# Optimization experiments

Measured on AMD Instinct MI355X. Metric: run time of the kernel, lower is better.

The kernel has to match this reference:

```python
import jax, jax.numpy as jnp
import numpy as np

EPS = 1e-4

def setup_inputs() -> dict:
    key = jax.random.key(0)
    x = jax.random.normal(key, (32, 512, 4000), dtype=jnp.float32)
    return {"x": x}

def reference(x):
    # x: [batch, bins, frames]; causal cumulative normalization along frames
    frames = x.shape[-1]
    count = jnp.arange(1, frames + 1, dtype=x.dtype).reshape(1, 1, frames)
    cum_sum = jnp.cumsum(x, axis=-1)
    cum_pow_sum = jnp.cumsum(x * x, axis=-1)
    cum_mean = cum_sum / count
    cum_var = cum_pow_sum / count - cum_mean * cum_mean
    cum_std = jnp.sqrt(cum_var + EPS)
    return (x - cum_mean) / cum_std
```

## Files before the change

### kernel.cpp

```cpp
#include <hip/hip_runtime.h>

#define EPS 1e-4f
#define FRAMES 4000

__global__ __launch_bounds__(256) void cumnorm_kernel(const float* __restrict__ x,
                                                      float* __restrict__ out,
                                                      int rows) {
    const int wavesPerBlock = blockDim.x >> 6;
    const int row  = blockIdx.x * wavesPerBlock + (threadIdx.x >> 6);
    const int lane = threadIdx.x & 63;
    if (row >= rows) return;

    const float4* __restrict__ xr = (const float4*)(x + (size_t)row * FRAMES);
    float4* __restrict__ outr     = (float4*)(out + (size_t)row * FRAMES);

    const int nvec = FRAMES >> 2;
    float carry_s = 0.0f, carry_q = 0.0f;

    for (int base = 0; base < nvec; base += 64) {
        const int idx = base + lane;
        float4 v = make_float4(0.0f, 0.0f, 0.0f, 0.0f);
        if (idx < nvec) v = xr[idx];

        float s0 = v.x;
        float s1 = s0 + v.y;
        float s2 = s1 + v.z;
        float s3 = s2 + v.w;
        float q0 = v.x * v.x;
        float q1 = fmaf(v.y, v.y, q0);
        float q2 = fmaf(v.z, v.z, q1);
        float q3 = fmaf(v.w, v.w, q2);

        float ss = s3, qq = q3;
        #pragma unroll
        for (int d = 1; d < 64; d <<= 1) {
            float us = __shfl_up(ss, d, 64);
            float uq = __shfl_up(qq, d, 64);
            if (lane >= d) { ss += us; qq += uq; }
        }

        const float tot_s = __shfl(ss, 63, 64);
        const float tot_q = __shfl(qq, 63, 64);

        const float excl_s = (ss - s3) + carry_s;
        const float excl_q = (qq - q3) + carry_q;

        if (idx < nvec) {
            const float base_cnt = (float)(idx << 2);
            float4 r;
            {
                const float cs = excl_s + s0, cq = excl_q + q0;
                const float inv  = __builtin_amdgcn_rcpf(base_cnt + 1.0f);
                const float mean = cs * inv;
                const float var  = fmaf(-mean, mean, cq * inv);
                r.x = (v.x - mean) * __builtin_amdgcn_rsqf(var + EPS);
            }
            {
                const float cs = excl_s + s1, cq = excl_q + q1;
                const float inv  = __builtin_amdgcn_rcpf(base_cnt + 2.0f);
                const float mean = cs * inv;
                const float var  = fmaf(-mean, mean, cq * inv);
                r.y = (v.y - mean) * __builtin_amdgcn_rsqf(var + EPS);
            }
            {
                const float cs = excl_s + s2, cq = excl_q + q2;
                const float inv  = __builtin_amdgcn_rcpf(base_cnt + 3.0f);
                const float mean = cs * inv;
                const float var  = fmaf(-mean, mean, cq * inv);
                r.z = (v.z - mean) * __builtin_amdgcn_rsqf(var + EPS);
            }
            {
                const float cs = excl_s + s3, cq = excl_q + q3;
                const float inv  = __builtin_amdgcn_rcpf(base_cnt + 4.0f);
                const float mean = cs * inv;
                const float var  = fmaf(-mean, mean, cq * inv);
                r.w = (v.w - mean) * __builtin_amdgcn_rsqf(var + EPS);
            }
            outr[idx] = r;
        }

        carry_s += tot_s;
        carry_q += tot_q;
    }
}

extern "C" void kernel_launch(void* const* d_in, const int* in_sizes, int n_in,
                              void* d_out, int out_size, void* d_ws, size_t ws_size,
                              hipStream_t stream) {
    const float* x = (const float*)d_in[0];
    float* out = (float*)d_out;
    const int rows = in_sizes[0] / FRAMES;

    const int block = 256;
    const int rowsPerBlock = block / 64;
    const int grid = (rows + rowsPerBlock - 1) / rowsPerBlock;
    cumnorm_kernel<<<grid, block, 0, stream>>>(x, out, rows);
}
```

Baseline: 432.6 us.

## Scan each row with a whole block using per-thread register chunks

Switches from one wave per row looping over 16 serial chunks to one 256-thread block per row. Each of the 250 active threads loads 16 contiguous elements, does a local serial sum, then a wave shuffle scan plus a shared-memory cross-wave combine. This removes the serial chunk loop and its carried dependency and exposes more memory parallelism per row. In exchange it adds a block barrier, leaves 6 threads idle, and has each thread load four contiguous float4s, which is a strided pattern across lanes.

```diff
diff --git a/kernel.cpp b/kernel.cpp
--- a/kernel.cpp
+++ b/kernel.cpp
@@ -2,85 +2,98 @@
 
 #define EPS 1e-4f
 #define FRAMES 4000
+#define TPB 256
+#define VPT 4
+#define EPT (VPT * 4)
+#define ACTIVE_T (FRAMES / EPT)
 
-__global__ __launch_bounds__(256) void cumnorm_kernel(const float* __restrict__ x,
+__global__ __launch_bounds__(TPB) void cumnorm_kernel(const float* __restrict__ x,
                                                       float* __restrict__ out,
                                                       int rows) {
-    const int wavesPerBlock = blockDim.x >> 6;
-    const int row  = blockIdx.x * wavesPerBlock + (threadIdx.x >> 6);
-    const int lane = threadIdx.x & 63;
+    const int row  = blockIdx.x;
     if (row >= rows) return;
+    const int t    = threadIdx.x;
+    const int wave = t >> 6;
+    const int lane = t & 63;
 
     const float4* __restrict__ xr = (const float4*)(x + (size_t)row * FRAMES);
     float4* __restrict__ outr     = (float4*)(out + (size_t)row * FRAMES);
 
-    const int nvec = FRAMES >> 2;
-    float carry_s = 0.0f, carry_q = 0.0f;
+    const bool active = (t < ACTIVE_T);
 
-    for (int base = 0; base < nvec; base += 64) {
-        const int idx = base + lane;
-        float4 v = make_float4(0.0f, 0.0f, 0.0f, 0.0f);
-        if (idx < nvec) v = xr[idx];
+    float4 v[VPT];
+    if (active) {
+        #pragma unroll
+        for (int j = 0; j < VPT; ++j) v[j] = xr[t * VPT + j];
+    } else {
+        #pragma unroll
+        for (int j = 0; j < VPT; ++j) v[j] = make_float4(0.f, 0.f, 0.f, 0.f);
+    }
 
-        float s0 = v.x;
-        float s1 = s0 + v.y;
-        float s2 = s1 + v.z;
-        float s3 = s2 + v.w;
-        float q0 = v.x * v.x;
-        float q1 = fmaf(v.y, v.y, q0);
-        float q2 = fmaf(v.z, v.z, q1);
-        float q3 = fmaf(v.w, v.w, q2);
+    float S = 0.f, Q = 0.f;
+    #pragma unroll
+    for (int j = 0; j < VPT; ++j) {
+        S += v[j].x; Q = fmaf(v[j].x, v[j].x, Q);
+        S += v[j].y; Q = fmaf(v[j].y, v[j].y, Q);
+        S += v[j].z; Q = fmaf(v[j].z, v[j].z, Q);
+        S += v[j].w; Q = fmaf(v[j].w, v[j].w, Q);
+    }
 
-        float ss = s3, qq = q3;
+    float ss = S, qq = Q;
+    #pragma unroll
+    for (int d = 1; d < 64; d <<= 1) {
+        const float us = __shfl_up(ss, d, 64);
+        const float uq = __shfl_up(qq, d, 64);
+        if (lane >= d) { ss += us; qq += uq; }
+    }
+
+    __shared__ float wsum[4];
+    __shared__ float wsq[4];
+    if (lane == 63) { wsum[wave] = ss; wsq[wave] = qq; }
+    __syncthreads();
+
+    float cs = ss - S;
+    float cq = qq - Q;
+    #pragma unroll
+    for (int w = 0; w < 3; ++w) {
+        if (w < wave) { cs += wsum[w]; cq += wsq[w]; }
+    }
+
+    if (active) {
+        const float nbase = (float)(t * EPT);
         #pragma unroll
-        for (int d = 1; d < 64; d <<= 1) {
-            float us = __shfl_up(ss, d, 64);
-            float uq = __shfl_up(qq, d, 64);
-            if (lane >= d) { ss += us; qq += uq; }
-        }
-
-        const float tot_s = __shfl(ss, 63, 64);
-        const float tot_q = __shfl(qq, 63, 64);
-
-        const float excl_s = (ss - s3) + carry_s;
-        const float excl_q = (qq - q3) + carry_q;
-
-        if (idx < nvec) {
-            const float base_cnt = (float)(idx << 2);
+        for (int j = 0; j < VPT; ++j) {
             float4 r;
             {
-                const float cs = excl_s + s0, cq = excl_q + q0;
-                const float inv  = __builtin_amdgcn_rcpf(base_cnt + 1.0f);
+                cs += v[j].x; cq = fmaf(v[j].x, v[j].x, cq);
+                const float inv  = __builtin_amdgcn_rcpf(nbase + (float)(j * 4 + 1));
                 const float mean = cs * inv;
                 const float var  = fmaf(-mean, mean, cq * inv);
-                r.x = (v.x - mean) * __builtin_amdgcn_rsqf(var + EPS);
+                r.x = (v[j].x - mean) * __builtin_amdgcn_rsqf(var + EPS);
             }
             {
-                const float cs = excl_s + s1, cq = excl_q + q1;
-                const float inv  = __builtin_amdgcn_rcpf(base_cnt + 2.0f);
+                cs += v[j].y; cq = fmaf(v[j].y, v[j].y, cq);
+                const float inv  = __builtin_amdgcn_rcpf(nbase + (float)(j * 4 + 2));
                 const float mean = cs * inv;
                 const float var  = fmaf(-mean, mean, cq * inv);
-                r.y = (v.y - mean) * __builtin_amdgcn_rsqf(var + EPS);
+                r.y = (v[j].y - mean) * __builtin_amdgcn_rsqf(var + EPS);
             }
             {
-                const float cs = excl_s + s2, cq = excl_q + q2;
-                const float inv  = __builtin_amdgcn_rcpf(base_cnt + 3.0f);
+                cs += v[j].z; cq = fmaf(v[j].z, v[j].z, cq);
+                const float inv  = __builtin_amdgcn_rcpf(nbase + (float)(j * 4 + 3));
                 const float mean = cs * inv;
                 const float var  = fmaf(-mean, mean, cq * inv);
-                r.z = (v.z - mean) * __builtin_amdgcn_rsqf(var + EPS);
+                r.z = (v[j].z - mean) * __builtin_amdgcn_rsqf(var + EPS);
             }
             {
-                const float cs = excl_s + s3, cq = excl_q + q3;
-                const float inv  = __builtin_amdgcn_rcpf(base_cnt + 4.0f);
+                cs += v[j].w; cq = fmaf(v[j].w, v[j].w, cq);
+                const float inv  = __builtin_amdgcn_rcpf(nbase + (float)(j * 4 + 4));
                 const float mean = cs * inv;
                 const float var  = fmaf(-mean, mean, cq * inv);
-                r.w = (v.w - mean) * __builtin_amdgcn_rsqf(var + EPS);
+                r.w = (v[j].w - mean) * __builtin_amdgcn_rsqf(var + EPS);
             }
-            outr[idx] = r;
+            outr[t * VPT + j] = r;
         }
-
-        carry_s += tot_s;
-        carry_q += tot_q;
     }
 }
 
@@ -91,8 +104,7 @@
     float* out = (float*)d_out;
     const int rows = in_sizes[0] / FRAMES;
 
-    const int block = 256;
-    const int rowsPerBlock = block / 64;
-    const int grid = (rows + rowsPerBlock - 1) / rowsPerBlock;
+    dim3 grid(rows);
+    dim3 block(TPB);
     cumnorm_kernel<<<grid, block, 0, stream>>>(x, out, rows);
 }
```

Measured after the change: 433.3 us. No clear change (+0.2%).
